# Kernel optimization log

Hardware: AMD Instinct MI355X
Metric: run time of the kernel (lower is better)

## Reference

```python
import jax, jax.numpy as jnp
import numpy as np

QMAX = 127.0  # int8 symmetric quantization range


def _quant_dequant(w):
    """Per-output-channel symmetric int8 fake quantization (weight-only),
    mimicking nn.quantized.Linear.from_float weight quantization."""
    scale = jnp.max(jnp.abs(w), axis=-1, keepdims=True) / QMAX
    scale = jnp.maximum(scale, 1e-8)
    q = jnp.clip(jnp.round(w / scale), -QMAX, QMAX)
    return q * scale


def setup_inputs() -> dict:
    key = jax.random.key(0)
    ks = jax.random.split(key, 7)
    B, S, D, F, E, NS = 2, 2048, 1024, 2048, 8, 1
    std = 1.0 / np.sqrt(D)
    x = jax.random.normal(ks[0], (B, S, D), dtype=jnp.float32)
    router_w = _quant_dequant(jax.random.normal(ks[1], (E, D), dtype=jnp.float32) * std)
    router_b = jnp.zeros((E,), dtype=jnp.float32)
    w_up = _quant_dequant(jax.random.normal(ks[2], (E, F, D), dtype=jnp.float32) * std)
    w_down = _quant_dequant(jax.random.normal(ks[3], (E, D, F), dtype=jnp.float32) / np.sqrt(F))
    shared_w_up = _quant_dequant(jax.random.normal(ks[4], (NS, F, D), dtype=jnp.float32) * std)
    shared_w_down = _quant_dequant(jax.random.normal(ks[5], (NS, D, F), dtype=jnp.float32) / np.sqrt(F))
    return {"x": x, "router_w": router_w, "router_b": router_b,
            "w_up": w_up, "w_down": w_down,
            "shared_w_up": shared_w_up, "shared_w_down": shared_w_down}


def reference(x, router_w, router_b, w_up, w_down, shared_w_up, shared_w_down):
    B, S, D = x.shape
    E = router_w.shape[0]
    TOPK = 2
    xt = x.reshape(-1, D)  # [T, D] tokens

    # Router (quantized linear) -> softmax -> top-k dispatch weights
    logits = xt @ router_w.T + router_b            # [T, E]
    probs = jax.nn.softmax(logits, axis=-1)        # [T, E]
    top_vals, top_idx = jax.lax.top_k(probs, TOPK)  # [T, K]
    top_vals = top_vals / jnp.sum(top_vals, axis=-1, keepdims=True)  # renormalize
    # combine[t, e] = routing weight of expert e for token t (0 if not selected)
    combine = jnp.sum(jax.nn.one_hot(top_idx, E, dtype=xt.dtype) * top_vals[..., None], axis=1)  # [T, E]

    # Routed experts: up -> SiLU -> down, computed densely then combined
    h = jnp.einsum('td,efd->tef', xt, w_up)        # [T, E, F]
    y = jnp.einsum('tef,edf->ted', jax.nn.silu(h), w_down)  # [T, E, D]
    out = jnp.einsum('ted,te->td', y, combine)     # [T, D]

    # Shared experts: always active, summed
    hs = jnp.einsum('td,sfd->tsf', xt, shared_w_up)          # [T, NS, F]
    out = out + jnp.einsum('tsf,sdf->td', jax.nn.silu(hs), shared_w_down)

    return out.reshape(B, S, D)
```

## Files before the change

kernel.cpp:

```cpp
#include <hip/hip_runtime.h>
#include <stdint.h>

typedef unsigned short u16;
typedef int i32x4 __attribute__((ext_vector_type(4)));
typedef unsigned int u32x4 __attribute__((ext_vector_type(4)));
typedef unsigned int u32x2 __attribute__((ext_vector_type(2)));

#define DDIM 1024
#define FDIM 2048
#define NEXP 8
#define RT_TILES 72
#define SHOFF 9216
#define RCAP 13312
#define NRT 104
#define UPROWS 16384
#define DNROWS 8192
#define UPTOT (UPROWS + FDIM)
#define DNTOT (DNROWS + DDIM)
#define UPT2 (UPTOT / 2)
#define WQ_NT (UPT2 + DNTOT)
#define WQ_NW 4096


__device__ inline float bf2f(u16 u) {
    union { unsigned int i; float f; } v; v.i = ((unsigned int)u) << 16; return v.f;
}
__device__ inline u16 f2bf(float f) {
    union { float f; unsigned int i; } v; v.f = f;
    unsigned int lsb = (v.i >> 16) & 1u;
    return (u16)((v.i + 0x7fffu + lsb) >> 16);
}
__device__ inline int q8(float v, float inv) {
    int x = (int)rintf(v * inv);
    return x < -127 ? -127 : (x > 127 ? 127 : x);
}
__device__ inline unsigned pack4(float a, float b, float c, float d, float inv) {
    return (unsigned)(q8(a, inv) & 255) | ((unsigned)(q8(b, inv) & 255) << 8) |
           ((unsigned)(q8(c, inv) & 255) << 16) | ((unsigned)(q8(d, inv) & 255) << 24);
}

__device__ inline u32x4 ntld16(const char* p) {
    return __builtin_nontemporal_load((const u32x4*)p);
}
__device__ inline u32x2 ntld8(const char* p) {
    return __builtin_nontemporal_load((const u32x2*)p);
}
__device__ inline void ntst8(char* p, u32x2 v) {
    __builtin_nontemporal_store(v, (u32x2*)p);
}

__device__ inline float absmax8(u32x4 p) {
    union { u32x4 v; u16 h[8]; } u; u.v = p;
    float m = fabsf(bf2f(u.h[0]));
    #pragma unroll
    for (int d = 1; d < 8; d++) m = fmaxf(m, fabsf(bf2f(u.h[d])));
    return m;
}
__device__ inline void store8(char* dst, u32x4 p, float inv) {
    union { u32x4 v; u16 h[8]; } u; u.v = p;
    u32x2 o;
    o[0] = pack4(bf2f(u.h[0]), bf2f(u.h[1]), bf2f(u.h[2]), bf2f(u.h[3]), inv);
    o[1] = pack4(bf2f(u.h[4]), bf2f(u.h[5]), bf2f(u.h[6]), bf2f(u.h[7]), inv);
    ntst8(dst, o);
}
__device__ inline float wredmax(float m) {
    #pragma unroll
    for (int off = 32; off > 0; off >>= 1) m = fmaxf(m, __shfl_xor(m, off, 64));
    return m;
}

typedef const __attribute__((address_space(1))) void gas_void;
typedef __attribute__((address_space(3))) void las_void;
#define GLL16(g, l) __builtin_amdgcn_global_load_lds((gas_void*)(g), (las_void*)(l), 16, 0, 0)

__global__ __launch_bounds__(256) void detect_kernel(
    const u16* __restrict__ x, int* __restrict__ meta)
{
    __shared__ int scnt;
    if (threadIdx.x == 0) scnt = 0;
    __syncthreads();
    int bad = 0;
    #pragma unroll
    for (int i = 0; i < 4; i++) {
        u16 v = x[threadIdx.x * 4 + i];
        if (((v >> 7) & 0xFF) >= 0x8F) bad++;
    }
    if (bad) atomicAdd(&scnt, bad);
    __syncthreads();
    if (threadIdx.x == 0) meta[30] = (scnt > 32) ? 1 : 0;
}

__global__ __launch_bounds__(256) void router_kernel(
    const void* __restrict__ x_, const void* __restrict__ rw_, const void* __restrict__ rb_,
    float* __restrict__ top_w, int* __restrict__ top_idx, const int* __restrict__ meta)
{
    __shared__ char smem[32768];
    const int tid = threadIdx.x;
    const int wave = tid >> 6, lane = tid & 63;
    const int flag = meta[30];

    float* rws = (float*)smem;
    if (!flag) {
        const ushort4* rwv = (const ushort4*)rw_;
        #pragma unroll
        for (int i = 0; i < 8; i++) {
            int idx = tid + i * 256;
            ushort4 h = rwv[idx];
            rws[idx * 4 + 0] = bf2f(h.x); rws[idx * 4 + 1] = bf2f(h.y);
            rws[idx * 4 + 2] = bf2f(h.z); rws[idx * 4 + 3] = bf2f(h.w);
        }
    } else {
        const float4* rwv = (const float4*)rw_;
        #pragma unroll
        for (int i = 0; i < 8; i++) {
            int idx = tid + i * 256;
            float4 f = rwv[idx];
            rws[idx * 4 + 0] = f.x; rws[idx * 4 + 1] = f.y;
            rws[idx * 4 + 2] = f.z; rws[idx * 4 + 3] = f.w;
        }
    }
    __syncthreads();

    for (int sub = 0; sub < 4; sub++) {
        const int t = blockIdx.x * 16 + wave * 4 + sub;
        float xv[16];
        if (!flag) {
            const u16* xr = (const u16*)x_ + (size_t)t * DDIM + lane * 16;
            uint4 p0 = *(const uint4*)(xr);
            uint4 p1 = *(const uint4*)(xr + 8);
            #pragma unroll
            for (int d = 0; d < 8; d++) xv[d]     = bf2f(((const u16*)&p0)[d]);
            #pragma unroll
            for (int d = 0; d < 8; d++) xv[d + 8] = bf2f(((const u16*)&p1)[d]);
        } else {
            const float4* xr = (const float4*)((const float*)x_ + (size_t)t * DDIM + lane * 16);
            #pragma unroll
            for (int c = 0; c < 4; c++) {
                float4 f = xr[c];
                xv[c * 4 + 0] = f.x; xv[c * 4 + 1] = f.y;
                xv[c * 4 + 2] = f.z; xv[c * 4 + 3] = f.w;
            }
        }
        float acc[NEXP];
        #pragma unroll
        for (int e = 0; e < NEXP; e++) {
            const float* wr = &rws[e * DDIM + lane * 16];
            float s = 0.f;
            #pragma unroll
            for (int d = 0; d < 16; d++) s += xv[d] * wr[d];
            acc[e] = s;
        }
        #pragma unroll
        for (int e = 0; e < NEXP; e++) {
            #pragma unroll
            for (int off = 32; off > 0; off >>= 1)
                acc[e] += __shfl_xor(acc[e], off, 64);
        }
        if (lane == 0) {
            float lg[NEXP];
            #pragma unroll
            for (int e = 0; e < NEXP; e++) {
                float b = flag ? ((const float*)rb_)[e] : bf2f(((const u16*)rb_)[e]);
                lg[e] = acc[e] + b;
            }
            int i0 = 0;
            #pragma unroll
            for (int e = 1; e < NEXP; e++) if (lg[e] > lg[i0]) i0 = e;
            int i1 = (i0 == 0) ? 1 : 0;
            #pragma unroll
            for (int e = 0; e < NEXP; e++) if (e != i0 && lg[e] > lg[i1]) i1 = e;
            float e1 = __expf(lg[i1] - lg[i0]);
            float w0 = 1.f / (1.f + e1);
            float w1 = e1 / (1.f + e1);
            top_w[2 * t] = w0;  top_w[2 * t + 1] = w1;
            top_idx[2 * t] = i0; top_idx[2 * t + 1] = i1;
        }
    }
}


__device__ inline const char* wq_src(int t, const char* wup, const char* swup,
                                     const char* wdn, const char* swdn) {
    if (t < UPT2) {
        const int R0 = t * 2;
        return (R0 < UPROWS) ? wup + (size_t)R0 * 2048
                             : swup + (size_t)(R0 - UPROWS) * 2048;
    }
    const int R = t - UPT2;
    return (R < DNROWS) ? wdn + (size_t)R * 4096
                        : swdn + (size_t)(R - DNROWS) * 4096;
}

template<int NC>
__device__ inline void wq_f32(const char* __restrict__ src, char* __restrict__ dst,
                              float* __restrict__ sout, int R, int lane) {
    float m = 0.f;
    #pragma unroll
    for (int c = 0; c < NC; c++) {
        float4 f = *(const float4*)(src + (size_t)c * 1024 + lane * 16);
        m = fmaxf(m, fmaxf(fmaxf(fabsf(f.x), fabsf(f.y)),
                           fmaxf(fabsf(f.z), fabsf(f.w))));
    }
    m = wredmax(m);
    m = fmaxf(m, 1e-12f);
    if (lane == 0) sout[R] = m / 127.f;
    const float inv = 127.f / m;
    #pragma unroll
    for (int c = 0; c < NC; c++) {
        float4 f = *(const float4*)(src + (size_t)c * 1024 + lane * 16);
        *(unsigned*)(dst + (size_t)c * 256 + lane * 4) = pack4(f.x, f.y, f.z, f.w, inv);
    }
}

__global__ __launch_bounds__(256) void wquant_kernel(
    const void* __restrict__ w_up, const void* __restrict__ w_down,
    const void* __restrict__ sw_up, const void* __restrict__ sw_down,
    char* __restrict__ qup, char* __restrict__ qdn,
    float* __restrict__ su, float* __restrict__ sd, const int* __restrict__ meta)
{
    const int gwid = (blockIdx.x * blockDim.x + threadIdx.x) >> 6;
    const int lane = threadIdx.x & 63;
    const int flag = meta[30];

    if (flag) {
        for (int t = gwid; t < WQ_NT; t += WQ_NW) {
            if (t < UPT2) {
                const int R0 = t * 2;
                const char* src = (R0 < UPROWS)
                    ? (const char*)w_up + (size_t)R0 * 4096
                    : (const char*)sw_up + (size_t)(R0 - UPROWS) * 4096;
                wq_f32<4>(src,        qup + (size_t)R0 * 1024,       su, R0,     lane);
                wq_f32<4>(src + 4096, qup + (size_t)(R0 + 1) * 1024, su, R0 + 1, lane);
            } else {
                const int R = t - UPT2;
                const char* src = (R < DNROWS)
                    ? (const char*)w_down + (size_t)R * 8192
                    : (const char*)sw_down + (size_t)(R - DNROWS) * 8192;
                wq_f32<8>(src, qdn + (size_t)R * 2048, sd, R, lane);
            }
        }
        return;
    }

    const char* wup  = (const char*)w_up;
    const char* swup = (const char*)sw_up;
    const char* wdn  = (const char*)w_down;
    const char* swdn = (const char*)sw_down;

    u32x4 A0, A1, A2, A3, B0, B1, B2, B3;

#define WQLOAD(P0, P1, P2, P3, T) do { \
        const char* s_ = wq_src((T), wup, swup, wdn, swdn); \
        P0 = ntld16(s_ + lane * 16); \
        P1 = ntld16(s_ + 1024 + lane * 16); \
        P2 = ntld16(s_ + 2048 + lane * 16); \
        P3 = ntld16(s_ + 3072 + lane * 16); \
    } while (0)

#define WQPROC(P0, P1, P2, P3, T) do { \
        if ((T) < UPT2) { \
            const int R0_ = (T) * 2; \
            float m0_ = fmaxf(absmax8(P0), absmax8(P1)); \
            float m1_ = fmaxf(absmax8(P2), absmax8(P3)); \
            m0_ = fmaxf(wredmax(m0_), 1e-12f); \
            m1_ = fmaxf(wredmax(m1_), 1e-12f); \
            if (lane == 0) { su[R0_] = m0_ / 127.f; su[R0_ + 1] = m1_ / 127.f; } \
            char* d_ = qup + (size_t)R0_ * 1024; \
            store8(d_ + lane * 8,        P0, 127.f / m0_); \
            store8(d_ + 512 + lane * 8,  P1, 127.f / m0_); \
            store8(d_ + 1024 + lane * 8, P2, 127.f / m1_); \
            store8(d_ + 1536 + lane * 8, P3, 127.f / m1_); \
        } else { \
            const int R_ = (T) - UPT2; \
            float m_ = fmaxf(fmaxf(absmax8(P0), absmax8(P1)), \
                             fmaxf(absmax8(P2), absmax8(P3))); \
            m_ = fmaxf(wredmax(m_), 1e-12f); \
            if (lane == 0) sd[R_] = m_ / 127.f; \
            const float inv_ = 127.f / m_; \
            char* d_ = qdn + (size_t)R_ * 2048; \
            store8(d_ + lane * 8,        P0, inv_); \
            store8(d_ + 512 + lane * 8,  P1, inv_); \
            store8(d_ + 1024 + lane * 8, P2, inv_); \
            store8(d_ + 1536 + lane * 8, P3, inv_); \
        } \
    } while (0)

    int tA = gwid;
    if (tA >= WQ_NT) return;
    WQLOAD(A0, A1, A2, A3, tA);
    while (true) {
        const int tB = tA + WQ_NW;
        if (tB < WQ_NT) {
            WQLOAD(B0, B1, B2, B3, tB);
            WQPROC(A0, A1, A2, A3, tA);
        } else {
            WQPROC(A0, A1, A2, A3, tA);
            return;
        }
        tA = tB + WQ_NW;
        if (tA < WQ_NT) {
            WQLOAD(A0, A1, A2, A3, tA);
            WQPROC(B0, B1, B2, B3, tB);
        } else {
            WQPROC(B0, B1, B2, B3, tB);
            return;
        }
    }
#undef WQLOAD
#undef WQPROC
}

__global__ __launch_bounds__(1024) void rank_kernel(
    const int* __restrict__ top_idx, int* __restrict__ tok_rows, int* __restrict__ meta)
{
    __shared__ int wsum[16][NEXP];
    __shared__ int wbase[16][NEXP];
    const int tid = threadIdx.x, lane = tid & 63, wave = tid >> 6;

    const int4* tp = (const int4*)(top_idx + tid * 8);
    int4 v0 = tp[0], v1 = tp[1];
    int e[8] = { v0.x, v0.y, v0.z, v0.w, v1.x, v1.y, v1.z, v1.w };

    int tcnt[NEXP];
    #pragma unroll
    for (int en = 0; en < NEXP; en++) tcnt[en] = 0;
    #pragma unroll
    for (int j = 0; j < 8; j++)
        #pragma unroll
        for (int en = 0; en < NEXP; en++) tcnt[en] += (e[j] == en);

    int excl[NEXP];
    #pragma unroll
    for (int en = 0; en < NEXP; en++) {
        int v = tcnt[en];
        #pragma unroll
        for (int off = 1; off < 64; off <<= 1) {
            int u = __shfl_up(v, off, 64);
            if (lane >= off) v += u;
        }
        excl[en] = v - tcnt[en];
        if (lane == 63) wsum[wave][en] = v;
    }
    __syncthreads();
    if (tid < NEXP) {
        int s = 0;
        for (int w = 0; w < 16; w++) { int c = wsum[w][tid]; wbase[w][tid] = s; s += c; }
        meta[tid] = s;
    }
    __syncthreads();
    if (tid == 0) {
        int b = 0;
        for (int en = 0; en < NEXP; en++) {
            meta[8 + en] = b;
            b += ((meta[en] + 127) >> 7) << 7;
        }
        meta[16] = b;
    }
    __syncthreads();

    int cur[NEXP];
    #pragma unroll
    for (int en = 0; en < NEXP; en++) cur[en] = meta[8 + en] + wbase[wave][en] + excl[en];

    int r[8];
    #pragma unroll
    for (int j = 0; j < 8; j++) {
        int rr = 0;
        #pragma unroll
        for (int en = 0; en < NEXP; en++)
            if (e[j] == en) { rr = cur[en]; cur[en] = rr + 1; }
        r[j] = rr;
    }
    int4* rp = (int4*)(tok_rows + tid * 8);
    rp[0] = make_int4(r[0], r[1], r[2], r[3]);
    rp[1] = make_int4(r[4], r[5], r[6], r[7]);
}

__global__ __launch_bounds__(128) void gather_q_kernel(
    const void* __restrict__ x_, const int* __restrict__ tok_rows,
    char* __restrict__ xq, float* __restrict__ sxa, const int* __restrict__ meta)
{
    __shared__ float wmax[2];
    const int t = blockIdx.x, tid = threadIdx.x;
    const int wave = tid >> 6, lane = tid & 63;
    const int r0 = tok_rows[2 * t], r1 = tok_rows[2 * t + 1];

    float v[8];
    if (!meta[30]) {
        u32x4 p = ntld16((const char*)x_ + (size_t)t * DDIM * 2 + tid * 16);
        union { u32x4 v; u16 h[8]; } u; u.v = p;
        #pragma unroll
        for (int d = 0; d < 8; d++) v[d] = bf2f(u.h[d]);
    } else {
        const float4* xf = (const float4*)((const float*)x_ + (size_t)t * DDIM);
        float4 a = xf[2 * tid], b = xf[2 * tid + 1];
        v[0] = a.x; v[1] = a.y; v[2] = a.z; v[3] = a.w;
        v[4] = b.x; v[5] = b.y; v[6] = b.z; v[7] = b.w;
    }
    float m = 0.f;
    #pragma unroll
    for (int d = 0; d < 8; d++) m = fmaxf(m, fabsf(v[d]));
    m = wredmax(m);
    if (lane == 0) wmax[wave] = m;
    __syncthreads();
    const float mx = fmaxf(fmaxf(wmax[0], wmax[1]), 1e-8f);
    const float inv = 127.f / mx;

    u32x2 u;
    u[0] = pack4(v[0], v[1], v[2], v[3], inv);
    u[1] = pack4(v[4], v[5], v[6], v[7], inv);

    ntst8(xq + (size_t)r0 * DDIM + tid * 8, u);
    ntst8(xq + (size_t)r1 * DDIM + tid * 8, u);
    ntst8(xq + (size_t)(SHOFF + t) * DDIM + tid * 8, u);
    if (tid == 0) {
        float s = mx / 127.f;
        sxa[r0] = s; sxa[r1] = s; sxa[SHOFF + t] = s;
    }
}

__global__ __launch_bounds__(256, 2) void moe_gemm_i8(
    const char* __restrict__ A, const char* __restrict__ Wq,
    const float* __restrict__ sa, const float* __restrict__ sw,
    u16* __restrict__ Cout, const int* __restrict__ meta, int N, int Kd, int act)
{
    const int L = blockIdx.y * gridDim.x + blockIdx.x;
    const int xcd = L & 7;
    const int jj = L >> 3;
    const int rt = xcd * 13 + (jj % 13);
    const int ct = jj / 13;

    int e;
    if (rt >= RT_TILES) {
        e = NEXP;
    } else {
        const int r0t = rt * 128;
        if (r0t >= meta[16]) return;
        e = 0;
        #pragma unroll
        for (int i = 1; i < NEXP; i++) if (r0t >= meta[8 + i]) e = i;
        if (r0t >= meta[8 + e] + meta[e]) return;
    }
    const char* Wb = Wq + (size_t)(e * N + ct * 128) * Kd;
    const float* swb = sw + e * N + ct * 128;

    __shared__ char As[2][128 * 64];
    __shared__ char Bs[2][128 * 64];

    const int tid = threadIdx.x;
    const int wave = tid >> 6, lane = tid & 63;
    const int wm = (wave >> 1) * 64;
    const int wn = (wave & 1) * 64;
    const int l16 = lane & 15;
    const int q = lane >> 4;
    const int slot = (q + (l16 >> 1)) & 3;

    const int rsub = lane >> 2;
    const int qs = ((lane & 3) - ((lane >> 3) & 3)) & 3;

    const char* Ag = A + (size_t)(rt * 128 + wave * 16 + rsub) * Kd + qs * 16;
    const char* Bg = Wb + (size_t)(wave * 16 + rsub) * Kd + qs * 16;
    const size_t rstep = (size_t)64 * Kd;

    i32x4 acc[4][4] = {};

#define STAGE(buf, off) do { \
        GLL16(Ag + (off),         &As[buf][wave * 1024]); \
        GLL16(Ag + (off) + rstep, &As[buf][4096 + wave * 1024]); \
        GLL16(Bg + (off),         &Bs[buf][wave * 1024]); \
        GLL16(Bg + (off) + rstep, &Bs[buf][4096 + wave * 1024]); \
    } while (0)

    STAGE(0, 0);
    __syncthreads();

    int cur = 0;
    for (int kk = 0; kk < Kd; kk += 64) {
        if (kk + 64 < Kd) STAGE(cur ^ 1, kk + 64);
        i32x4 af[4], bf[4];
        #pragma unroll
        for (int i = 0; i < 4; i++)
            af[i] = *(const i32x4*)&As[cur][(wm + i * 16 + l16) * 64 + slot * 16];
        #pragma unroll
        for (int j = 0; j < 4; j++)
            bf[j] = *(const i32x4*)&Bs[cur][(wn + j * 16 + l16) * 64 + slot * 16];
        #pragma unroll
        for (int i = 0; i < 4; i++)
            #pragma unroll
            for (int j = 0; j < 4; j++)
                acc[i][j] = __builtin_amdgcn_mfma_i32_16x16x64_i8(af[i], bf[j], acc[i][j], 0, 0, 0);
        __syncthreads();
        cur ^= 1;
    }
#undef STAGE

    float sal[4][4];
    #pragma unroll
    for (int i = 0; i < 4; i++)
        #pragma unroll
        for (int rr = 0; rr < 4; rr++)
            sal[i][rr] = sa[rt * 128 + wm + i * 16 + q * 4 + rr];
    float swl[4];
    #pragma unroll
    for (int j = 0; j < 4; j++) swl[j] = swb[wn + j * 16 + l16];

    u16* Crow = Cout + (size_t)(rt * 128) * N + ct * 128;
    #pragma unroll
    for (int i = 0; i < 4; i++) {
        #pragma unroll
        for (int j = 0; j < 4; j++) {
            #pragma unroll
            for (int rr = 0; rr < 4; rr++) {
                const int row = wm + i * 16 + q * 4 + rr;
                const int col = wn + j * 16 + l16;
                float v = (float)acc[i][j][rr] * sal[i][rr] * swl[j];
                if (act) v = v / (1.f + __expf(-v));
                Crow[(size_t)row * N + col] = f2bf(v);
            }
        }
    }
}

__global__ __launch_bounds__(256) void hquant_kernel(
    const u16* __restrict__ hg, char* __restrict__ h8, float* __restrict__ sh,
    const int* __restrict__ meta)
{
    const int gwid = (blockIdx.x * blockDim.x + threadIdx.x) >> 6;
    const int lane = threadIdx.x & 63;
    const int m16 = meta[16];
    const int NT = m16 + (RCAP - SHOFF);
    const int gap = SHOFF - m16;
    if (gwid >= NT) return;

    u32x4 A0, A1, A2, A3, B0, B1, B2, B3;

#define HROW(T) ((T) < m16 ? (T) : (T) + gap)
#define HLOAD(P0, P1, P2, P3, T) do { \
        const char* r_ = (const char*)(hg + (size_t)HROW(T) * FDIM); \
        P0 = ntld16(r_ + lane * 16); \
        P1 = ntld16(r_ + 1024 + lane * 16); \
        P2 = ntld16(r_ + 2048 + lane * 16); \
        P3 = ntld16(r_ + 3072 + lane * 16); \
    } while (0)
#define HPROC(P0, P1, P2, P3, T) do { \
        const int r_ = HROW(T); \
        float m_ = fmaxf(fmaxf(absmax8(P0), absmax8(P1)), \
                         fmaxf(absmax8(P2), absmax8(P3))); \
        m_ = fmaxf(wredmax(m_), 1e-8f); \
        if (lane == 0) sh[r_] = m_ / 127.f; \
        const float inv_ = 127.f / m_; \
        char* d_ = h8 + (size_t)r_ * FDIM; \
        store8(d_ + lane * 8,        P0, inv_); \
        store8(d_ + 512 + lane * 8,  P1, inv_); \
        store8(d_ + 1024 + lane * 8, P2, inv_); \
        store8(d_ + 1536 + lane * 8, P3, inv_); \
    } while (0)

    int tA = gwid;
    HLOAD(A0, A1, A2, A3, tA);
    while (true) {
        const int tB = tA + WQ_NW;
        if (tB < NT) {
            HLOAD(B0, B1, B2, B3, tB);
            HPROC(A0, A1, A2, A3, tA);
        } else {
            HPROC(A0, A1, A2, A3, tA);
            return;
        }
        tA = tB + WQ_NW;
        if (tA < NT) {
            HLOAD(A0, A1, A2, A3, tA);
            HPROC(B0, B1, B2, B3, tB);
        } else {
            HPROC(B0, B1, B2, B3, tB);
            return;
        }
    }
#undef HROW
#undef HLOAD
#undef HPROC
}

__global__ __launch_bounds__(256) void combine_kernel(
    const u16* __restrict__ yg, const float* __restrict__ top_w,
    const int* __restrict__ tok_rows, void* __restrict__ out_, const int* __restrict__ meta)
{
    const int t = blockIdx.x;
    const int r0 = tok_rows[2 * t], r1 = tok_rows[2 * t + 1];
    const float w0 = top_w[2 * t], w1 = top_w[2 * t + 1];
    const int d = threadIdx.x * 4;
    union { u32x2 v; u16 h[4]; } y0, y1, ys;
    y0.v = ntld8((const char*)(yg + (size_t)r0 * DDIM + d));
    y1.v = ntld8((const char*)(yg + (size_t)r1 * DDIM + d));
    ys.v = ntld8((const char*)(yg + (size_t)(SHOFF + t) * DDIM + d));
    float o0 = w0 * bf2f(y0.h[0]) + w1 * bf2f(y1.h[0]) + bf2f(ys.h[0]);
    float o1 = w0 * bf2f(y0.h[1]) + w1 * bf2f(y1.h[1]) + bf2f(ys.h[1]);
    float o2 = w0 * bf2f(y0.h[2]) + w1 * bf2f(y1.h[2]) + bf2f(ys.h[2]);
    float o3 = w0 * bf2f(y0.h[3]) + w1 * bf2f(y1.h[3]) + bf2f(ys.h[3]);
    if (!meta[30]) {
        union { u32x2 v; u16 h[4]; } o;
        o.h[0] = f2bf(o0); o.h[1] = f2bf(o1); o.h[2] = f2bf(o2); o.h[3] = f2bf(o3);
        ntst8((char*)((u16*)out_ + (size_t)t * DDIM + d), o.v);
    } else {
        float4 o; o.x = o0; o.y = o1; o.z = o2; o.w = o3;
        *(float4*)((float*)out_ + (size_t)t * DDIM + d) = o;
    }
}

extern "C" void kernel_launch(void* const* d_in, const int* in_sizes, int n_in,
                              void* d_out, int out_size, void* d_ws, size_t ws_size,
                              hipStream_t stream) {
    const void* x       = d_in[0];
    const void* rw      = d_in[1];
    const void* rb      = d_in[2];
    const void* w_up    = d_in[3];
    const void* w_down  = d_in[4];
    const void* sw_up   = d_in[5];
    const void* sw_down = d_in[6];

    const int T = in_sizes[0] / DDIM;

    char* ws = (char*)d_ws;
    int*   meta     = (int*)ws;
    float* top_w    = (float*)(ws + 1024);
    int*   top_idx  = (int*)(ws + 1024 + 8 * T);
    int*   tok_rows = (int*)(ws + 1024 + 16 * T);
    size_t off = 131072;
    u16*  yg = (u16*)(ws + off);
    char* xq = (char*)(ws + off);
    off += (size_t)RCAP * DDIM * 2;
    u16*  hg = (u16*)(ws + off);
    off += (size_t)RCAP * FDIM * 2;
    char* h8 = (char*)(ws + off);
    off += (size_t)RCAP * FDIM;
    char* qup = (char*)(ws + off);
    off += (size_t)(NEXP + 1) * FDIM * DDIM;
    char* qdn = (char*)(ws + off);
    off += (size_t)(NEXP + 1) * DDIM * FDIM;
    float* sxa = (float*)(ws + off); off += (size_t)RCAP * 4;
    float* sh  = (float*)(ws + off); off += (size_t)RCAP * 4;
    float* su  = (float*)(ws + off); off += (size_t)(NEXP + 1) * FDIM * 4;
    float* sd  = (float*)(ws + off); off += (size_t)(NEXP + 1) * DDIM * 4;

    detect_kernel<<<1, 256, 0, stream>>>((const u16*)x, meta);

    const int nrb = T / 16;
    router_kernel<<<nrb, 256, 0, stream>>>(x, rw, rb, top_w, top_idx, meta);
    wquant_kernel<<<WQ_NW / 4, 256, 0, stream>>>(
        w_up, w_down, sw_up, sw_down, qup, qdn, su, sd, meta);
    rank_kernel<<<1, 1024, 0, stream>>>(top_idx, tok_rows, meta);
    gather_q_kernel<<<T, 128, 0, stream>>>(x, tok_rows, xq, sxa, meta);

    moe_gemm_i8<<<dim3(FDIM / 128, NRT), 256, 0, stream>>>(
        xq, qup, sxa, su, hg, meta, FDIM, DDIM, 1);
    hquant_kernel<<<WQ_NW / 4, 256, 0, stream>>>(hg, h8, sh, meta);
    moe_gemm_i8<<<dim3(DDIM / 128, NRT), 256, 0, stream>>>(
        h8, qdn, sh, sd, yg, meta, DDIM, FDIM, 0);
    combine_kernel<<<T, 256, 0, stream>>>(yg, top_w, tok_rows, d_out, meta);
}
```

Baseline: 326.3 us.

## Fuse router with up-weight quant and overlap down-weight quant with up GEMM

Removes the standalone detect kernel and inlines dtype detection into each consumer. The router now runs in the same launch as up-projection weight quantization, and down-projection weight quantization shares a launch with the up GEMM, using extra blocks past the GEMM tiles. The intent is to cut launch count and let memory-bound quantization overlap compute-bound GEMM work. Costs include repeated detection work in every block, a dedicated up-GEMM copy with a hardcoded XCD-aware tile mapping, and the removal of software double-buffering in the quant loops.

```diff
diff --git a/kernel.cpp b/kernel.cpp
--- a/kernel.cpp
+++ b/kernel.cpp
@@ -18,8 +18,8 @@
 #define UPTOT (UPROWS + FDIM)
 #define DNTOT (DNROWS + DDIM)
 #define UPT2 (UPTOT / 2)
-#define WQ_NT (UPT2 + DNTOT)
-#define WQ_NW 4096
+#define WQW 4608
+#define NG_UP 1664
 
 
 __device__ inline float bf2f(u16 u) {
@@ -73,122 +73,18 @@
 typedef __attribute__((address_space(3))) void las_void;
 #define GLL16(g, l) __builtin_amdgcn_global_load_lds((gas_void*)(g), (las_void*)(l), 16, 0, 0)
 
-__global__ __launch_bounds__(256) void detect_kernel(
-    const u16* __restrict__ x, int* __restrict__ meta)
-{
-    __shared__ int scnt;
-    if (threadIdx.x == 0) scnt = 0;
-    __syncthreads();
+__device__ inline int detect_inline(const u16* __restrict__ x, int* sh) {
+    if (threadIdx.x == 0) *sh = 0;
+    __syncthreads();
+    const int per = 1024 / blockDim.x;
     int bad = 0;
-    #pragma unroll
-    for (int i = 0; i < 4; i++) {
-        u16 v = x[threadIdx.x * 4 + i];
+    for (int i = 0; i < per; i++) {
+        u16 v = x[threadIdx.x * per + i];
         if (((v >> 7) & 0xFF) >= 0x8F) bad++;
     }
-    if (bad) atomicAdd(&scnt, bad);
-    __syncthreads();
-    if (threadIdx.x == 0) meta[30] = (scnt > 32) ? 1 : 0;
-}
-
-__global__ __launch_bounds__(256) void router_kernel(
-    const void* __restrict__ x_, const void* __restrict__ rw_, const void* __restrict__ rb_,
-    float* __restrict__ top_w, int* __restrict__ top_idx, const int* __restrict__ meta)
-{
-    __shared__ char smem[32768];
-    const int tid = threadIdx.x;
-    const int wave = tid >> 6, lane = tid & 63;
-    const int flag = meta[30];
-
-    float* rws = (float*)smem;
-    if (!flag) {
-        const ushort4* rwv = (const ushort4*)rw_;
-        #pragma unroll
-        for (int i = 0; i < 8; i++) {
-            int idx = tid + i * 256;
-            ushort4 h = rwv[idx];
-            rws[idx * 4 + 0] = bf2f(h.x); rws[idx * 4 + 1] = bf2f(h.y);
-            rws[idx * 4 + 2] = bf2f(h.z); rws[idx * 4 + 3] = bf2f(h.w);
-        }
-    } else {
-        const float4* rwv = (const float4*)rw_;
-        #pragma unroll
-        for (int i = 0; i < 8; i++) {
-            int idx = tid + i * 256;
-            float4 f = rwv[idx];
-            rws[idx * 4 + 0] = f.x; rws[idx * 4 + 1] = f.y;
-            rws[idx * 4 + 2] = f.z; rws[idx * 4 + 3] = f.w;
-        }
-    }
-    __syncthreads();
-
-    for (int sub = 0; sub < 4; sub++) {
-        const int t = blockIdx.x * 16 + wave * 4 + sub;
-        float xv[16];
-        if (!flag) {
-            const u16* xr = (const u16*)x_ + (size_t)t * DDIM + lane * 16;
-            uint4 p0 = *(const uint4*)(xr);
-            uint4 p1 = *(const uint4*)(xr + 8);
-            #pragma unroll
-            for (int d = 0; d < 8; d++) xv[d]     = bf2f(((const u16*)&p0)[d]);
-            #pragma unroll
-            for (int d = 0; d < 8; d++) xv[d + 8] = bf2f(((const u16*)&p1)[d]);
-        } else {
-            const float4* xr = (const float4*)((const float*)x_ + (size_t)t * DDIM + lane * 16);
-            #pragma unroll
-            for (int c = 0; c < 4; c++) {
-                float4 f = xr[c];
-                xv[c * 4 + 0] = f.x; xv[c * 4 + 1] = f.y;
-                xv[c * 4 + 2] = f.z; xv[c * 4 + 3] = f.w;
-            }
-        }
-        float acc[NEXP];
-        #pragma unroll
-        for (int e = 0; e < NEXP; e++) {
-            const float* wr = &rws[e * DDIM + lane * 16];
-            float s = 0.f;
-            #pragma unroll
-            for (int d = 0; d < 16; d++) s += xv[d] * wr[d];
-            acc[e] = s;
-        }
-        #pragma unroll
-        for (int e = 0; e < NEXP; e++) {
-            #pragma unroll
-            for (int off = 32; off > 0; off >>= 1)
-                acc[e] += __shfl_xor(acc[e], off, 64);
-        }
-        if (lane == 0) {
-            float lg[NEXP];
-            #pragma unroll
-            for (int e = 0; e < NEXP; e++) {
-                float b = flag ? ((const float*)rb_)[e] : bf2f(((const u16*)rb_)[e]);
-                lg[e] = acc[e] + b;
-            }
-            int i0 = 0;
-            #pragma unroll
-            for (int e = 1; e < NEXP; e++) if (lg[e] > lg[i0]) i0 = e;
-            int i1 = (i0 == 0) ? 1 : 0;
-            #pragma unroll
-            for (int e = 0; e < NEXP; e++) if (e != i0 && lg[e] > lg[i1]) i1 = e;
-            float e1 = __expf(lg[i1] - lg[i0]);
-            float w0 = 1.f / (1.f + e1);
-            float w1 = e1 / (1.f + e1);
-            top_w[2 * t] = w0;  top_w[2 * t + 1] = w1;
-            top_idx[2 * t] = i0; top_idx[2 * t + 1] = i1;
-        }
-    }
-}
-
-
-__device__ inline const char* wq_src(int t, const char* wup, const char* swup,
-                                     const char* wdn, const char* swdn) {
-    if (t < UPT2) {
-        const int R0 = t * 2;
-        return (R0 < UPROWS) ? wup + (size_t)R0 * 2048
-                             : swup + (size_t)(R0 - UPROWS) * 2048;
-    }
-    const int R = t - UPT2;
-    return (R < DNROWS) ? wdn + (size_t)R * 4096
-                        : swdn + (size_t)(R - DNROWS) * 4096;
+    if (bad) atomicAdd(sh, bad);
+    __syncthreads();
+    return (*sh > 32) ? 1 : 0;
 }
 
 template<int NC>
@@ -212,110 +108,143 @@
     }
 }
 
-__global__ __launch_bounds__(256) void wquant_kernel(
-    const void* __restrict__ w_up, const void* __restrict__ w_down,
-    const void* __restrict__ sw_up, const void* __restrict__ sw_down,
-    char* __restrict__ qup, char* __restrict__ qdn,
-    float* __restrict__ su, float* __restrict__ sd, const int* __restrict__ meta)
+__global__ __launch_bounds__(256) void fused_rw_kernel(
+    const void* __restrict__ x_, const void* __restrict__ rw_, const void* __restrict__ rb_,
+    const void* __restrict__ w_up, const void* __restrict__ sw_up,
+    float* __restrict__ top_w, int* __restrict__ top_idx,
+    char* __restrict__ qup, float* __restrict__ su, int nrb)
 {
-    const int gwid = (blockIdx.x * blockDim.x + threadIdx.x) >> 6;
-    const int lane = threadIdx.x & 63;
-    const int flag = meta[30];
-
-    if (flag) {
-        for (int t = gwid; t < WQ_NT; t += WQ_NW) {
-            if (t < UPT2) {
-                const int R0 = t * 2;
-                const char* src = (R0 < UPROWS)
-                    ? (const char*)w_up + (size_t)R0 * 4096
-                    : (const char*)sw_up + (size_t)(R0 - UPROWS) * 4096;
-                wq_f32<4>(src,        qup + (size_t)R0 * 1024,       su, R0,     lane);
-                wq_f32<4>(src + 4096, qup + (size_t)(R0 + 1) * 1024, su, R0 + 1, lane);
+    __shared__ char smem[32768 + 16];
+    const int tid = threadIdx.x;
+    const int wave = tid >> 6, lane = tid & 63;
+    const int flag = detect_inline((const u16*)x_, (int*)(smem + 32768));
+
+    if ((int)blockIdx.x < nrb) {
+        float* rws = (float*)smem;
+        if (!flag) {
+            const ushort4* rwv = (const ushort4*)rw_;
+            #pragma unroll
+            for (int i = 0; i < 8; i++) {
+                int idx = tid + i * 256;
+                ushort4 h = rwv[idx];
+                rws[idx * 4 + 0] = bf2f(h.x); rws[idx * 4 + 1] = bf2f(h.y);
+                rws[idx * 4 + 2] = bf2f(h.z); rws[idx * 4 + 3] = bf2f(h.w);
+            }
+        } else {
+            const float4* rwv = (const float4*)rw_;
+            #pragma unroll
+            for (int i = 0; i < 8; i++) {
+                int idx = tid + i * 256;
+                float4 f = rwv[idx];
+                rws[idx * 4 + 0] = f.x; rws[idx * 4 + 1] = f.y;
+                rws[idx * 4 + 2] = f.z; rws[idx * 4 + 3] = f.w;
+            }
+        }
+        __syncthreads();
+
+        for (int sub = 0; sub < 4; sub++) {
+            const int t = blockIdx.x * 16 + wave * 4 + sub;
+            float xv[16];
+            if (!flag) {
+                const u16* xr = (const u16*)x_ + (size_t)t * DDIM + lane * 16;
+                uint4 p0 = *(const uint4*)(xr);
+                uint4 p1 = *(const uint4*)(xr + 8);
+                #pragma unroll
+                for (int d = 0; d < 8; d++) xv[d]     = bf2f(((const u16*)&p0)[d]);
+                #pragma unroll
+                for (int d = 0; d < 8; d++) xv[d + 8] = bf2f(((const u16*)&p1)[d]);
             } else {
-                const int R = t - UPT2;
-                const char* src = (R < DNROWS)
-                    ? (const char*)w_down + (size_t)R * 8192
-                    : (const char*)sw_down + (size_t)(R - DNROWS) * 8192;
-                wq_f32<8>(src, qdn + (size_t)R * 2048, sd, R, lane);
+                const float4* xr = (const float4*)((const float*)x_ + (size_t)t * DDIM + lane * 16);
+                #pragma unroll
+                for (int c = 0; c < 4; c++) {
+                    float4 f = xr[c];
+                    xv[c * 4 + 0] = f.x; xv[c * 4 + 1] = f.y;
+                    xv[c * 4 + 2] = f.z; xv[c * 4 + 3] = f.w;
+                }
+            }
+            float acc[NEXP];
+            #pragma unroll
+            for (int e = 0; e < NEXP; e++) {
+                const float* wr = &rws[e * DDIM + lane * 16];
+                float s = 0.f;
+                #pragma unroll
+                for (int d = 0; d < 16; d++) s += xv[d] * wr[d];
+                acc[e] = s;
+            }
+            #pragma unroll
+            for (int e = 0; e < NEXP; e++) {
+                #pragma unroll
+                for (int off = 32; off > 0; off >>= 1)
+                    acc[e] += __shfl_xor(acc[e], off, 64);
+            }
+            if (lane == 0) {
+                float lg[NEXP];
+                #pragma unroll
+                for (int e = 0; e < NEXP; e++) {
+                    float b = flag ? ((const float*)rb_)[e] : bf2f(((const u16*)rb_)[e]);
+                    lg[e] = acc[e] + b;
+                }
+                int i0 = 0;
+                #pragma unroll
+                for (int e = 1; e < NEXP; e++) if (lg[e] > lg[i0]) i0 = e;
+                int i1 = (i0 == 0) ? 1 : 0;
+                #pragma unroll
+                for (int e = 0; e < NEXP; e++) if (e != i0 && lg[e] > lg[i1]) i1 = e;
+                float e1 = __expf(lg[i1] - lg[i0]);
+                float w0 = 1.f / (1.f + e1);
+                float w1 = e1 / (1.f + e1);
+                top_w[2 * t] = w0;  top_w[2 * t + 1] = w1;
+                top_idx[2 * t] = i0; top_idx[2 * t + 1] = i1;
             }
         }
         return;
     }
 
-    const char* wup  = (const char*)w_up;
-    const char* swup = (const char*)sw_up;
-    const char* wdn  = (const char*)w_down;
-    const char* swdn = (const char*)sw_down;
-
-    u32x4 A0, A1, A2, A3, B0, B1, B2, B3;
-
-#define WQLOAD(P0, P1, P2, P3, T) do { \
-        const char* s_ = wq_src((T), wup, swup, wdn, swdn); \
-        P0 = ntld16(s_ + lane * 16); \
-        P1 = ntld16(s_ + 1024 + lane * 16); \
-        P2 = ntld16(s_ + 2048 + lane * 16); \
-        P3 = ntld16(s_ + 3072 + lane * 16); \
-    } while (0)
-
-#define WQPROC(P0, P1, P2, P3, T) do { \
-        if ((T) < UPT2) { \
-            const int R0_ = (T) * 2; \
-            float m0_ = fmaxf(absmax8(P0), absmax8(P1)); \
-            float m1_ = fmaxf(absmax8(P2), absmax8(P3)); \
-            m0_ = fmaxf(wredmax(m0_), 1e-12f); \
-            m1_ = fmaxf(wredmax(m1_), 1e-12f); \
-            if (lane == 0) { su[R0_] = m0_ / 127.f; su[R0_ + 1] = m1_ / 127.f; } \
-            char* d_ = qup + (size_t)R0_ * 1024; \
-            store8(d_ + lane * 8,        P0, 127.f / m0_); \
-            store8(d_ + 512 + lane * 8,  P1, 127.f / m0_); \
-            store8(d_ + 1024 + lane * 8, P2, 127.f / m1_); \
-            store8(d_ + 1536 + lane * 8, P3, 127.f / m1_); \
-        } else { \
-            const int R_ = (T) - UPT2; \
-            float m_ = fmaxf(fmaxf(absmax8(P0), absmax8(P1)), \
-                             fmaxf(absmax8(P2), absmax8(P3))); \
-            m_ = fmaxf(wredmax(m_), 1e-12f); \
-            if (lane == 0) sd[R_] = m_ / 127.f; \
-            const float inv_ = 127.f / m_; \
-            char* d_ = qdn + (size_t)R_ * 2048; \
-            store8(d_ + lane * 8,        P0, inv_); \
-            store8(d_ + 512 + lane * 8,  P1, inv_); \
-            store8(d_ + 1024 + lane * 8, P2, inv_); \
-            store8(d_ + 1536 + lane * 8, P3, inv_); \
-        } \
-    } while (0)
-
-    int tA = gwid;
-    if (tA >= WQ_NT) return;
-    WQLOAD(A0, A1, A2, A3, tA);
-    while (true) {
-        const int tB = tA + WQ_NW;
-        if (tB < WQ_NT) {
-            WQLOAD(B0, B1, B2, B3, tB);
-            WQPROC(A0, A1, A2, A3, tA);
-        } else {
-            WQPROC(A0, A1, A2, A3, tA);
-            return;
-        }
-        tA = tB + WQ_NW;
-        if (tA < WQ_NT) {
-            WQLOAD(A0, A1, A2, A3, tA);
-            WQPROC(B0, B1, B2, B3, tB);
-        } else {
-            WQPROC(B0, B1, B2, B3, tB);
-            return;
-        }
-    }
-#undef WQLOAD
-#undef WQPROC
+    const int gwid = ((int)blockIdx.x - nrb) * 4 + wave;
+    if (!flag) {
+        for (int t = gwid; t < UPT2; t += WQW) {
+            const int R0 = t * 2;
+            const char* src = (R0 < UPROWS)
+                ? (const char*)w_up + (size_t)R0 * 2048
+                : (const char*)sw_up + (size_t)(R0 - UPROWS) * 2048;
+            u32x4 P0 = ntld16(src + lane * 16);
+            u32x4 P1 = ntld16(src + 1024 + lane * 16);
+            u32x4 P2 = ntld16(src + 2048 + lane * 16);
+            u32x4 P3 = ntld16(src + 3072 + lane * 16);
+            float m0 = fmaxf(absmax8(P0), absmax8(P1));
+            float m1 = fmaxf(absmax8(P2), absmax8(P3));
+            m0 = fmaxf(wredmax(m0), 1e-12f);
+            m1 = fmaxf(wredmax(m1), 1e-12f);
+            if (lane == 0) { su[R0] = m0 / 127.f; su[R0 + 1] = m1 / 127.f; }
+            char* d = qup + (size_t)R0 * 1024;
+            store8(d + lane * 8,        P0, 127.f / m0);
+            store8(d + 512 + lane * 8,  P1, 127.f / m0);
+            store8(d + 1024 + lane * 8, P2, 127.f / m1);
+            store8(d + 1536 + lane * 8, P3, 127.f / m1);
+        }
+    } else {
+        for (int t = gwid; t < UPT2; t += WQW) {
+            const int R0 = t * 2;
+            const char* src = (R0 < UPROWS)
+                ? (const char*)w_up + (size_t)R0 * 4096
+                : (const char*)sw_up + (size_t)(R0 - UPROWS) * 4096;
+            wq_f32<4>(src,        qup + (size_t)R0 * 1024,       su, R0,     lane);
+            wq_f32<4>(src + 4096, qup + (size_t)(R0 + 1) * 1024, su, R0 + 1, lane);
+        }
+    }
 }
 
 __global__ __launch_bounds__(1024) void rank_kernel(
-    const int* __restrict__ top_idx, int* __restrict__ tok_rows, int* __restrict__ meta)
+    const u16* __restrict__ x, const int* __restrict__ top_idx,
+    int* __restrict__ tok_rows, int* __restrict__ meta)
 {
     __shared__ int wsum[16][NEXP];
     __shared__ int wbase[16][NEXP];
+    __shared__ int scnt;
     const int tid = threadIdx.x, lane = tid & 63, wave = tid >> 6;
+
+    const int flag = detect_inline(x, &scnt);
+    if (tid == 0) meta[30] = flag;
 
     const int4* tp = (const int4*)(top_idx + tid * 8);
     int4 v0 = tp[0], v1 = tp[1];
@@ -416,6 +345,145 @@
     if (tid == 0) {
         float s = mx / 127.f;
         sxa[r0] = s; sxa[r1] = s; sxa[SHOFF + t] = s;
+    }
+}
+
+__global__ __launch_bounds__(256, 2) void gemm_up_wqdn(
+    const char* __restrict__ A, const char* __restrict__ Wq,
+    const float* __restrict__ sa, const float* __restrict__ sw,
+    u16* __restrict__ Cout, const int* __restrict__ meta,
+    const void* __restrict__ w_down, const void* __restrict__ sw_down,
+    char* __restrict__ qdn, float* __restrict__ sd)
+{
+    __shared__ char As[2][128 * 64];
+    __shared__ char Bs[2][128 * 64];
+
+    const int bid = blockIdx.x;
+    const int tid = threadIdx.x;
+    const int wave = tid >> 6, lane = tid & 63;
+
+    if (bid >= NG_UP) {
+        const int gwid = (bid - NG_UP) * 4 + wave;
+        const int flag = meta[30];
+        if (!flag) {
+            for (int R = gwid; R < DNTOT; R += WQW) {
+                const char* src = (R < DNROWS)
+                    ? (const char*)w_down + (size_t)R * 4096
+                    : (const char*)sw_down + (size_t)(R - DNROWS) * 4096;
+                u32x4 P0 = ntld16(src + lane * 16);
+                u32x4 P1 = ntld16(src + 1024 + lane * 16);
+                u32x4 P2 = ntld16(src + 2048 + lane * 16);
+                u32x4 P3 = ntld16(src + 3072 + lane * 16);
+                float m = fmaxf(fmaxf(absmax8(P0), absmax8(P1)),
+                                fmaxf(absmax8(P2), absmax8(P3)));
+                m = fmaxf(wredmax(m), 1e-12f);
+                if (lane == 0) sd[R] = m / 127.f;
+                const float inv = 127.f / m;
+                char* d = qdn + (size_t)R * 2048;
+                store8(d + lane * 8,        P0, inv);
+                store8(d + 512 + lane * 8,  P1, inv);
+                store8(d + 1024 + lane * 8, P2, inv);
+                store8(d + 1536 + lane * 8, P3, inv);
+            }
+        } else {
+            for (int R = gwid; R < DNTOT; R += WQW) {
+                const char* src = (R < DNROWS)
+                    ? (const char*)w_down + (size_t)R * 8192
+                    : (const char*)sw_down + (size_t)(R - DNROWS) * 8192;
+                wq_f32<8>(src, qdn + (size_t)R * 2048, sd, R, lane);
+            }
+        }
+        return;
+    }
+
+    const int xcd = bid & 7;
+    const int jj = bid >> 3;
+    const int rt = xcd * 13 + (jj % 13);
+    const int ct = jj / 13;
+
+    int e;
+    if (rt >= RT_TILES) {
+        e = NEXP;
+    } else {
+        const int r0t = rt * 128;
+        if (r0t >= meta[16]) return;
+        e = 0;
+        #pragma unroll
+        for (int i = 1; i < NEXP; i++) if (r0t >= meta[8 + i]) e = i;
+        if (r0t >= meta[8 + e] + meta[e]) return;
+    }
+    const char* Wb = Wq + (size_t)(e * FDIM + ct * 128) * DDIM;
+    const float* swb = sw + e * FDIM + ct * 128;
+
+    const int wm = (wave >> 1) * 64;
+    const int wn = (wave & 1) * 64;
+    const int l16 = lane & 15;
+    const int q = lane >> 4;
+    const int slot = (q + (l16 >> 1)) & 3;
+
+    const int rsub = lane >> 2;
+    const int qs = ((lane & 3) - ((lane >> 3) & 3)) & 3;
+
+    const char* Ag = A + (size_t)(rt * 128 + wave * 16 + rsub) * DDIM + qs * 16;
+    const char* Bg = Wb + (size_t)(wave * 16 + rsub) * DDIM + qs * 16;
+    const size_t rstep = (size_t)64 * DDIM;
+
+    i32x4 acc[4][4] = {};
+
+#define STAGE(buf, off) do { \
+        GLL16(Ag + (off),         &As[buf][wave * 1024]); \
+        GLL16(Ag + (off) + rstep, &As[buf][4096 + wave * 1024]); \
+        GLL16(Bg + (off),         &Bs[buf][wave * 1024]); \
+        GLL16(Bg + (off) + rstep, &Bs[buf][4096 + wave * 1024]); \
+    } while (0)
+
+    STAGE(0, 0);
+    __syncthreads();
+
+    int cur = 0;
+    for (int kk = 0; kk < DDIM; kk += 64) {
+        if (kk + 64 < DDIM) STAGE(cur ^ 1, kk + 64);
+        i32x4 af[4], bf[4];
+        #pragma unroll
+        for (int i = 0; i < 4; i++)
+            af[i] = *(const i32x4*)&As[cur][(wm + i * 16 + l16) * 64 + slot * 16];
+        #pragma unroll
+        for (int j = 0; j < 4; j++)
+            bf[j] = *(const i32x4*)&Bs[cur][(wn + j * 16 + l16) * 64 + slot * 16];
+        #pragma unroll
+        for (int i = 0; i < 4; i++)
+            #pragma unroll
+            for (int j = 0; j < 4; j++)
+                acc[i][j] = __builtin_amdgcn_mfma_i32_16x16x64_i8(af[i], bf[j], acc[i][j], 0, 0, 0);
+        __syncthreads();
+        cur ^= 1;
+    }
+#undef STAGE
+
+    float sal[4][4];
+    #pragma unroll
+    for (int i = 0; i < 4; i++)
+        #pragma unroll
+        for (int rr = 0; rr < 4; rr++)
+            sal[i][rr] = sa[rt * 128 + wm + i * 16 + q * 4 + rr];
+    float swl[4];
+    #pragma unroll
+    for (int j = 0; j < 4; j++) swl[j] = swb[wn + j * 16 + l16];
+
+    u16* Crow = Cout + (size_t)(rt * 128) * FDIM + ct * 128;
+    #pragma unroll
+    for (int i = 0; i < 4; i++) {
+        #pragma unroll
+        for (int j = 0; j < 4; j++) {
+            #pragma unroll
+            for (int rr = 0; rr < 4; rr++) {
+                const int row = wm + i * 16 + q * 4 + rr;
+                const int col = wn + j * 16 + l16;
+                float v = (float)acc[i][j][rr] * sal[i][rr] * swl[j];
+                v = v / (1.f + __expf(-v));
+                Crow[(size_t)row * FDIM + col] = f2bf(v);
+            }
+        }
     }
 }
 
@@ -530,55 +598,25 @@
     const int m16 = meta[16];
     const int NT = m16 + (RCAP - SHOFF);
     const int gap = SHOFF - m16;
-    if (gwid >= NT) return;
-
-    u32x4 A0, A1, A2, A3, B0, B1, B2, B3;
-
-#define HROW(T) ((T) < m16 ? (T) : (T) + gap)
-#define HLOAD(P0, P1, P2, P3, T) do { \
-        const char* r_ = (const char*)(hg + (size_t)HROW(T) * FDIM); \
-        P0 = ntld16(r_ + lane * 16); \
-        P1 = ntld16(r_ + 1024 + lane * 16); \
-        P2 = ntld16(r_ + 2048 + lane * 16); \
-        P3 = ntld16(r_ + 3072 + lane * 16); \
-    } while (0)
-#define HPROC(P0, P1, P2, P3, T) do { \
-        const int r_ = HROW(T); \
-        float m_ = fmaxf(fmaxf(absmax8(P0), absmax8(P1)), \
-                         fmaxf(absmax8(P2), absmax8(P3))); \
-        m_ = fmaxf(wredmax(m_), 1e-8f); \
-        if (lane == 0) sh[r_] = m_ / 127.f; \
-        const float inv_ = 127.f / m_; \
-        char* d_ = h8 + (size_t)r_ * FDIM; \
-        store8(d_ + lane * 8,        P0, inv_); \
-        store8(d_ + 512 + lane * 8,  P1, inv_); \
-        store8(d_ + 1024 + lane * 8, P2, inv_); \
-        store8(d_ + 1536 + lane * 8, P3, inv_); \
-    } while (0)
-
-    int tA = gwid;
-    HLOAD(A0, A1, A2, A3, tA);
-    while (true) {
-        const int tB = tA + WQ_NW;
-        if (tB < NT) {
-            HLOAD(B0, B1, B2, B3, tB);
-            HPROC(A0, A1, A2, A3, tA);
-        } else {
-            HPROC(A0, A1, A2, A3, tA);
-            return;
-        }
-        tA = tB + WQ_NW;
-        if (tA < NT) {
-            HLOAD(A0, A1, A2, A3, tA);
-            HPROC(B0, B1, B2, B3, tB);
-        } else {
-            HPROC(B0, B1, B2, B3, tB);
-            return;
-        }
-    }
-#undef HROW
-#undef HLOAD
-#undef HPROC
+
+    for (int t = gwid; t < NT; t += 4096) {
+        const int r = (t < m16) ? t : t + gap;
+        const char* src = (const char*)(hg + (size_t)r * FDIM);
+        u32x4 P0 = ntld16(src + lane * 16);
+        u32x4 P1 = ntld16(src + 1024 + lane * 16);
+        u32x4 P2 = ntld16(src + 2048 + lane * 16);
+        u32x4 P3 = ntld16(src + 3072 + lane * 16);
+        float m = fmaxf(fmaxf(absmax8(P0), absmax8(P1)),
+                        fmaxf(absmax8(P2), absmax8(P3)));
+        m = fmaxf(wredmax(m), 1e-8f);
+        if (lane == 0) sh[r] = m / 127.f;
+        const float inv = 127.f / m;
+        char* d = h8 + (size_t)r * FDIM;
+        store8(d + lane * 8,        P0, inv);
+        store8(d + 512 + lane * 8,  P1, inv);
+        store8(d + 1024 + lane * 8, P2, inv);
+        store8(d + 1536 + lane * 8, P3, inv);
+    }
 }
 
 __global__ __launch_bounds__(256) void combine_kernel(
@@ -642,18 +680,14 @@
     float* su  = (float*)(ws + off); off += (size_t)(NEXP + 1) * FDIM * 4;
     float* sd  = (float*)(ws + off); off += (size_t)(NEXP + 1) * DDIM * 4;
 
-    detect_kernel<<<1, 256, 0, stream>>>((const u16*)x, meta);
-
     const int nrb = T / 16;
-    router_kernel<<<nrb, 256, 0, stream>>>(x, rw, rb, top_w, top_idx, meta);
-    wquant_kernel<<<WQ_NW / 4, 256, 0, stream>>>(
-        w_up, w_down, sw_up, sw_down, qup, qdn, su, sd, meta);
-    rank_kernel<<<1, 1024, 0, stream>>>(top_idx, tok_rows, meta);
+    fused_rw_kernel<<<nrb + 1152, 256, 0, stream>>>(
+        x, rw, rb, w_up, sw_up, top_w, top_idx, qup, su, nrb);
+    rank_kernel<<<1, 1024, 0, stream>>>((const u16*)x, top_idx, tok_rows, meta);
     gather_q_kernel<<<T, 128, 0, stream>>>(x, tok_rows, xq, sxa, meta);
-
-    moe_gemm_i8<<<dim3(FDIM / 128, NRT), 256, 0, stream>>>(
-        xq, qup, sxa, su, hg, meta, FDIM, DDIM, 1);
-    hquant_kernel<<<WQ_NW / 4, 256, 0, stream>>>(hg, h8, sh, meta);
+    gemm_up_wqdn<<<NG_UP + 1152, 256, 0, stream>>>(
+        xq, qup, sxa, su, hg, meta, w_down, sw_down, qdn, sd);
+    hquant_kernel<<<1024, 256, 0, stream>>>(hg, h8, sh, meta);
     moe_gemm_i8<<<dim3(DDIM / 128, NRT), 256, 0, stream>>>(
         h8, qdn, sh, sd, yg, meta, DDIM, FDIM, 0);
     combine_kernel<<<T, 256, 0, stream>>>(yg, top_w, tok_rows, d_out, meta);
```

Measured after the change: 311.0 us. -4.7%, faster.
